# Kernel tuning notes

Measured on AMD Instinct MI355X. Metric: run time of the kernel, lower is better.

The kernel has to match this reference:

```python
import jax, jax.numpy as jnp
import numpy as np

S, N, B, EMB = 20, 102400, 1024, 64


def setup_inputs() -> dict:
    key = jax.random.key(0)
    ks = jax.random.split(key, 8)
    nodes_abs = jax.random.normal(ks[0], (S, N, 2), jnp.float32) * 5.0
    nodes_norm = jax.random.normal(ks[1], (S, N, 2), jnp.float32)
    shift_value = jax.random.normal(ks[2], (S, N, 2), jnp.float32)
    seq_list = jax.random.uniform(ks[3], (S, N), jnp.float32) - 0.02
    scenes = jnp.arange(B, dtype=jnp.int32)
    pednum = jnp.full((B,), N // B, dtype=jnp.int32)  # peds per scene
    # TSModel stand-in parameters (2 -> EMB -> 2 with GM-history mixing)
    W_in = jax.random.normal(ks[4], (2, EMB), jnp.float32) * 0.5
    W_gm = jax.random.normal(ks[5], (EMB, EMB), jnp.float32) * (1.0 / np.sqrt(EMB))
    b_h = jnp.zeros((EMB,), jnp.float32)
    W_out = jax.random.normal(ks[6], (EMB, 2), jnp.float32) * (1.0 / np.sqrt(EMB))
    b_out = jnp.zeros((2,), jnp.float32)
    return {"nodes_abs": nodes_abs, "nodes_norm": nodes_norm, "shift_value": shift_value,
            "seq_list": seq_list, "scenes": scenes, "pednum": pednum,
            "W_in": W_in, "W_gm": W_gm, "b_h": b_h, "W_out": W_out, "b_out": b_out}


def reference(nodes_abs, nodes_norm, shift_value, seq_list, scenes, pednum,
              W_in, W_gm, b_h, W_out, b_out):
    S_, N_, _ = nodes_abs.shape
    B_ = pednum.shape[0]
    # scene id per pedestrian from cumsum(pednum) -- replaces get_st_ed slices
    scene_ids = jnp.searchsorted(jnp.cumsum(pednum), jnp.arange(N_), side="right")
    presence = seq_list > 0

    def step(carry, xs):
        mask, gm_sum = carry            # mask: [N] peds present in all frames 0..f
        pres_f, abs_f, f = xs
        mask = mask & pres_f            # get_node_index(seq_list[:f+1])
        mf = mask.astype(abs_f.dtype)   # [N]
        # center_alignment_spa: per-scene mean over active peds at frame f
        cnt = jax.ops.segment_sum(mf, scene_ids, num_segments=B_)
        ssum = jax.ops.segment_sum(abs_f * mf[:, None], scene_ids, num_segments=B_)
        center = ssum / jnp.maximum(cnt, 1.0)[:, None]            # [B,2]
        coord = (abs_f - center[scene_ids]) * mf[:, None]         # [N,2]
        # TSModel stand-in: embed centered coord + running GM-history mean
        gm_mean = gm_sum / jnp.maximum(f, 1).astype(gm_sum.dtype)  # mean of GM[:f]
        h = jnp.tanh(coord @ W_in + gm_mean @ W_gm + b_h) * mf[:, None]  # [N,EMB]
        out = (h @ W_out + b_out) * mf[:, None]                    # masked scatter write
        return (mask, gm_sum + h), out

    mask0 = jnp.ones((N_,), dtype=bool)
    gm0 = jnp.zeros((N_, W_gm.shape[0]), nodes_abs.dtype)
    xs = (presence[: S_ - 1], nodes_abs[: S_ - 1], jnp.arange(S_ - 1))
    _, outs = jax.lax.scan(step, (mask0, gm0), xs)                # [S-1,N,2]
    outputs = jnp.concatenate([outs, jnp.zeros((1, N_, 2), outs.dtype)], axis=0)
    return outputs
```

## Files before the change

### kernel.cpp

```cpp
#include <hip/hip_runtime.h>

#define S_DIM 20
#define NSTEP 19
#define EMB   64
#define GSTR  36
#define MAXP  128

typedef __attribute__((ext_vector_type(8))) short bf16x8;
typedef __attribute__((ext_vector_type(4))) float f32x4;

__device__ __forceinline__ uint32_t pk_bf16(float lo, float hi) {
    uint32_t r;
    asm("v_cvt_pk_bf16_f32 %0, %1, %2" : "=v"(r) : "v"(lo), "v"(hi));
    return r;
}
__device__ __forceinline__ short bf16s(float v) { return (short)(pk_bf16(v, v) & 0xffffu); }
__device__ __forceinline__ float unbf16(uint32_t lo16) {
    union { uint32_t u; float f; } c; c.u = lo16 << 16; return c.f;
}

__global__ __launch_bounds__(512, 4) void pfa_kernel(
    const float* __restrict__ nodes_abs,
    const float* __restrict__ seq_list,
    const int*   __restrict__ pednum,
    const float* __restrict__ W_in,
    const float* __restrict__ W_gm,
    const float* __restrict__ b_h,
    const float* __restrict__ W_out,
    const float* __restrict__ b_out,
    float*       __restrict__ out,
    int N, int B)
{
    const int b    = blockIdx.x;
    const int t    = threadIdx.x;
    const int lane = t & 63;
    const int w    = t >> 6;
    const int l15  = lane & 15;
    const int hi   = lane >> 4;

    __shared__ __attribute__((aligned(16))) uint32_t G[8 * 16 * GSTR];
    __shared__ uint32_t masks[MAXP];
    __shared__ float2   cxy[NSTEP];

    int partial = 0;
    for (int i = lane; i < b; i += 64) partial += pednum[i];
    #pragma unroll
    for (int off = 32; off; off >>= 1) partial += __shfl_xor(partial, off, 64);
    const int start = partial;
    const int P = min(pednum[b], MAXP);
    const int q = (P + 7) >> 3;

    {
        uint4* g4 = (uint4*)&G[w * 16 * GSTR];
        for (int i = lane; i < 16 * GSTR / 4; i += 64)
            g4[i] = make_uint4(0u, 0u, 0u, 0u);
    }

    bf16x8 agm[4][2];
    #pragma unroll
    for (int m = 0; m < 4; ++m)
        #pragma unroll
        for (int T = 0; T < 2; ++T)
            #pragma unroll
            for (int e = 0; e < 8; ++e)
                agm[m][T][e] = bf16s(W_gm[(32*T + 8*hi + e) * EMB + 16*m + l15]);

    bf16x8 aaug[4];
    #pragma unroll
    for (int m = 0; m < 4; ++m) {
        bf16x8 a = {0,0,0,0,0,0,0,0};
        if (hi == 0) {
            const int j = 16*m + l15;
            const float w0 = W_in[j], w1 = W_in[EMB + j], bh = b_h[j];
            const short w0h = bf16s(w0); const short w0l = bf16s(w0 - unbf16((uint16_t)w0h));
            const short w1h = bf16s(w1); const short w1l = bf16s(w1 - unbf16((uint16_t)w1h));
            const short bhh = bf16s(bh); const short bhl = bf16s(bh - unbf16((uint16_t)bhh));
            a[0]=w0h; a[1]=w0l; a[2]=w0h; a[3]=w1h; a[4]=w1l; a[5]=w1h; a[6]=bhh; a[7]=bhl;
        }
        aaug[m] = a;
    }

    bf16x8 aout[2];
    #pragma unroll
    for (int T = 0; T < 2; ++T)
        #pragma unroll
        for (int e = 0; e < 8; ++e) {
            const int j = 32*T + 8*hi + e;
            aout[T][e] = (l15 < 2) ? bf16s(W_out[j*2 + l15]) : (short)0;
        }
    const float bo0 = b_out[0], bo1 = b_out[1];

    if (t < P) {
        uint32_t m = 0; bool alive = true;
        #pragma unroll
        for (int f = 0; f < NSTEP; ++f) {
            alive = alive && (seq_list[(size_t)f * N + start + t] > 0.0f);
            m |= (alive ? 1u : 0u) << f;
        }
        masks[t] = m;
    }
    __syncthreads();

    for (int f = w; f < NSTEP; f += 8) {
        float cnt = 0.f, sx = 0.f, sy = 0.f;
        for (int p = lane; p < P; p += 64) {
            const float mf = (float)((masks[p] >> f) & 1u);
            const float2 a = *(const float2*)&nodes_abs[((size_t)f * N + start + p) * 2];
            cnt += mf; sx = fmaf(a.x, mf, sx); sy = fmaf(a.y, mf, sy);
        }
        #pragma unroll
        for (int off = 32; off; off >>= 1) {
            cnt += __shfl_xor(cnt, off, 64);
            sx  += __shfl_xor(sx , off, 64);
            sy  += __shfl_xor(sy , off, 64);
        }
        if (lane == 0) {
            const float ic = __builtin_amdgcn_rcpf(fmaxf(cnt, 1.0f));
            cxy[f] = make_float2(sx * ic, sy * ic);
        }
    }
    __syncthreads();

    const int  pd = w * q + l15;
    const bool vr = (l15 < q) && (pd < P);
    const int  gi = start + (vr ? pd : 0);
    const uint32_t mk = vr ? masks[pd] : 0u;
    float2 ab = *(const float2*)&nodes_abs[(size_t)gi * 2];

    uint32_t* const Grow = &G[(w * 16 + l15) * GSTR];
    const bool h0 = (hi == 0);

    f32x4 gm[4];
    const f32x4 zero4 = {0.f, 0.f, 0.f, 0.f};
    #pragma unroll
    for (int m = 0; m < 4; ++m) gm[m] = zero4;

    #pragma unroll 1
    for (int f = 0; f < NSTEP; ++f) {
        const float2 c = cxy[f];
        const float mf  = (float)((mk >> f) & 1u);
        const float cxd = ab.x - c.x;
        const float cyd = ab.y - c.y;
        ab = *(const float2*)&nodes_abs[((size_t)(f + 1) * N + gi) * 2];

        const uint32_t e0 = pk_bf16(cxd, cxd);
        const float    cxl = cxd - unbf16(e0 & 0xffffu);
        const uint32_t ey = pk_bf16(cyd, cyd);
        const float    cyl = cyd - unbf16(ey & 0xffffu);
        const uint32_t e1 = pk_bf16(cxl, cyd);
        const uint32_t e2 = pk_bf16(cyd, cyl);
        union { uint32_t u[4]; bf16x8 v; } b2u;
        b2u.u[0] = h0 ? e0 : 0u;
        b2u.u[1] = h0 ? e1 : 0u;
        b2u.u[2] = h0 ? e2 : 0u;
        b2u.u[3] = h0 ? 0x3f803f80u : 0u;

        const bf16x8 B0 = *(const bf16x8*)&Grow[ 0 + 4*hi];
        const bf16x8 B1 = *(const bf16x8*)&Grow[16 + 4*hi];

        f32x4 acc[4];
        #pragma unroll
        for (int m = 0; m < 4; ++m) {
            f32x4 cacc = zero4;
            cacc = __builtin_amdgcn_mfma_f32_16x16x32_bf16(aaug[m],   b2u.v, cacc, 0, 0, 0);
            cacc = __builtin_amdgcn_mfma_f32_16x16x32_bf16(agm[m][0], B0,    cacc, 0, 0, 0);
            cacc = __builtin_amdgcn_mfma_f32_16x16x32_bf16(agm[m][1], B1,    cacc, 0, 0, 0);
            acc[m] = cacc;
        }

        const float m2 = -2.0f * mf;
        #pragma unroll
        for (int m = 0; m < 4; ++m) {
            f32x4 h4;
            #pragma unroll
            for (int rr = 0; rr < 4; ++rr) {
                const float x  = acc[m][rr];
                const float e  = __expf(2.0f * x);
                const float tt = __builtin_amdgcn_rcpf(e + 1.0f);
                h4[rr] = fmaf(tt, m2, mf);
            }
            gm[m] += h4;
            const uint32_t p0 = pk_bf16(h4[0], h4[1]);
            const uint32_t p1 = pk_bf16(h4[2], h4[3]);
            *(uint2*)&Grow[8*m + 2*hi] = make_uint2(p0, p1);
        }

        const bf16x8 H0 = *(const bf16x8*)&Grow[ 0 + 4*hi];
        const bf16x8 H1 = *(const bf16x8*)&Grow[16 + 4*hi];
        f32x4 oc = zero4;
        oc = __builtin_amdgcn_mfma_f32_16x16x32_bf16(aout[0], H0, oc, 0, 0, 0);
        oc = __builtin_amdgcn_mfma_f32_16x16x32_bf16(aout[1], H1, oc, 0, 0, 0);
        if (h0 && vr) {
            float2 o;
            o.x = (oc[0] + bo0) * mf;
            o.y = (oc[1] + bo1) * mf;
            *(float2*)&out[((size_t)f * N + gi) * 2] = o;
        }

        const float invf2 = __builtin_amdgcn_rcpf((float)(f + 1));
        #pragma unroll
        for (int m = 0; m < 4; ++m) {
            const uint32_t p0 = pk_bf16(gm[m][0] * invf2, gm[m][1] * invf2);
            const uint32_t p1 = pk_bf16(gm[m][2] * invf2, gm[m][3] * invf2);
            *(uint2*)&Grow[8*m + 2*hi] = make_uint2(p0, p1);
        }
    }

    if (t < P) {
        const size_t o = ((size_t)(S_DIM - 1) * N + start + t) * 2;
        out[o] = 0.0f; out[o + 1] = 0.0f;
    }
}

extern "C" void kernel_launch(void* const* d_in, const int* in_sizes, int n_in,
                              void* d_out, int out_size, void* d_ws, size_t ws_size,
                              hipStream_t stream) {
    const float* nodes_abs = (const float*)d_in[0];
    const float* seq_list  = (const float*)d_in[3];
    const int*   pednum    = (const int*)  d_in[5];
    const float* W_in      = (const float*)d_in[6];
    const float* W_gm      = (const float*)d_in[7];
    const float* b_h       = (const float*)d_in[8];
    const float* W_out     = (const float*)d_in[9];
    const float* b_out     = (const float*)d_in[10];
    float*       out       = (float*)d_out;

    const int N = in_sizes[3] / S_DIM;
    const int B = in_sizes[5];

    pfa_kernel<<<B, 512, 0, stream>>>(nodes_abs, seq_list, pednum,
                                      W_in, W_gm, b_h, W_out, b_out,
                                      out, N, B);
}
```

Baseline: 87.63 us.

## Fuse output projection into tanh loop and store raw GM sums

```diff
diff --git a/kernel.cpp b/kernel.cpp
--- a/kernel.cpp
+++ b/kernel.cpp
@@ -80,13 +80,13 @@
         aaug[m] = a;
     }
 
-    bf16x8 aout[2];
-    #pragma unroll
-    for (int T = 0; T < 2; ++T)
-        #pragma unroll
-        for (int e = 0; e < 8; ++e) {
-            const int j = 32*T + 8*hi + e;
-            aout[T][e] = (l15 < 2) ? bf16s(W_out[j*2 + l15]) : (short)0;
+    f32x4 wo0[4], wo1[4];
+    #pragma unroll
+    for (int m = 0; m < 4; ++m)
+        #pragma unroll
+        for (int rr = 0; rr < 4; ++rr) {
+            const float2 v = *(const float2*)&W_out[(16*m + 4*hi + rr) * 2];
+            wo0[m][rr] = v.x; wo1[m][rr] = v.y;
         }
     const float bo0 = b_out[0], bo1 = b_out[1];
 
@@ -158,51 +158,41 @@
         const bf16x8 B0 = *(const bf16x8*)&Grow[ 0 + 4*hi];
         const bf16x8 B1 = *(const bf16x8*)&Grow[16 + 4*hi];
 
-        f32x4 acc[4];
+        const float invf = __builtin_amdgcn_rcpf((float)(f ? f : 1));
+        const float m2 = -2.0f * mf;
+
+        float o0 = 0.0f, o1 = 0.0f;
         #pragma unroll
         for (int m = 0; m < 4; ++m) {
-            f32x4 cacc = zero4;
-            cacc = __builtin_amdgcn_mfma_f32_16x16x32_bf16(aaug[m],   b2u.v, cacc, 0, 0, 0);
-            cacc = __builtin_amdgcn_mfma_f32_16x16x32_bf16(agm[m][0], B0,    cacc, 0, 0, 0);
-            cacc = __builtin_amdgcn_mfma_f32_16x16x32_bf16(agm[m][1], B1,    cacc, 0, 0, 0);
-            acc[m] = cacc;
-        }
-
-        const float m2 = -2.0f * mf;
-        #pragma unroll
-        for (int m = 0; m < 4; ++m) {
+            f32x4 ag = zero4;
+            ag = __builtin_amdgcn_mfma_f32_16x16x32_bf16(agm[m][0], B0, ag, 0, 0, 0);
+            ag = __builtin_amdgcn_mfma_f32_16x16x32_bf16(agm[m][1], B1, ag, 0, 0, 0);
+            f32x4 aa = zero4;
+            aa = __builtin_amdgcn_mfma_f32_16x16x32_bf16(aaug[m], b2u.v, aa, 0, 0, 0);
+
             f32x4 h4;
             #pragma unroll
             for (int rr = 0; rr < 4; ++rr) {
-                const float x  = acc[m][rr];
+                const float x  = fmaf(ag[rr], invf, aa[rr]);
                 const float e  = __expf(2.0f * x);
                 const float tt = __builtin_amdgcn_rcpf(e + 1.0f);
                 h4[rr] = fmaf(tt, m2, mf);
+                o0 = fmaf(h4[rr], wo0[m][rr], o0);
+                o1 = fmaf(h4[rr], wo1[m][rr], o1);
             }
             gm[m] += h4;
-            const uint32_t p0 = pk_bf16(h4[0], h4[1]);
-            const uint32_t p1 = pk_bf16(h4[2], h4[3]);
+            const uint32_t p0 = pk_bf16(gm[m][0], gm[m][1]);
+            const uint32_t p1 = pk_bf16(gm[m][2], gm[m][3]);
             *(uint2*)&Grow[8*m + 2*hi] = make_uint2(p0, p1);
         }
 
-        const bf16x8 H0 = *(const bf16x8*)&Grow[ 0 + 4*hi];
-        const bf16x8 H1 = *(const bf16x8*)&Grow[16 + 4*hi];
-        f32x4 oc = zero4;
-        oc = __builtin_amdgcn_mfma_f32_16x16x32_bf16(aout[0], H0, oc, 0, 0, 0);
-        oc = __builtin_amdgcn_mfma_f32_16x16x32_bf16(aout[1], H1, oc, 0, 0, 0);
+        o0 += __shfl_xor(o0, 16, 64);  o0 += __shfl_xor(o0, 32, 64);
+        o1 += __shfl_xor(o1, 16, 64);  o1 += __shfl_xor(o1, 32, 64);
         if (h0 && vr) {
             float2 o;
-            o.x = (oc[0] + bo0) * mf;
-            o.y = (oc[1] + bo1) * mf;
+            o.x = (o0 + bo0) * mf;
+            o.y = (o1 + bo1) * mf;
             *(float2*)&out[((size_t)f * N + gi) * 2] = o;
-        }
-
-        const float invf2 = __builtin_amdgcn_rcpf((float)(f + 1));
-        #pragma unroll
-        for (int m = 0; m < 4; ++m) {
-            const uint32_t p0 = pk_bf16(gm[m][0] * invf2, gm[m][1] * invf2);
-            const uint32_t p1 = pk_bf16(gm[m][2] * invf2, gm[m][3] * invf2);
-            *(uint2*)&Grow[8*m + 2*hi] = make_uint2(p0, p1);
         }
     }
 
```

New measurement: 103.7 us. +18.4%, slower.
